# Kernel optimization log

Measured on AMD Instinct MI355X. Metric: run time of the kernel, lower is better.

The kernel has to match this reference:

```python
import jax, jax.numpy as jnp
import numpy as np

STRIDE, PAD, DIL = 1, 1, 1

def setup_inputs() -> dict:
    key = jax.random.key(0)
    k1, k2, k3, k4, k5 = jax.random.split(key, 5)
    B, C, H, W = 4, 64, 96, 96
    Co, kh, kw = 64, 3, 3
    K = kh * kw
    return {
        "input": jax.random.normal(k1, (B, C, H, W), dtype=jnp.float32),
        "offset": jax.random.normal(k2, (B, 2 * K, H, W), dtype=jnp.float32),
        "mask": jax.random.uniform(k3, (B, K, H, W), dtype=jnp.float32),
        "weight": jax.random.normal(k4, (Co, C, kh, kw), dtype=jnp.float32) * 0.05,
        "bias": jax.random.normal(k5, (Co,), dtype=jnp.float32),
    }


def _dcnv2(input, offset, mask, weight, bias):
    B, C, H, W = input.shape
    Co, Ci, kh, kw = weight.shape
    K = kh * kw
    G = offset.shape[1] // (2 * K)  # deformable groups
    Cg = C // G
    Ho = (H + 2 * PAD - DIL * (kh - 1) - 1) // STRIDE + 1
    Wo = (W + 2 * PAD - DIL * (kw - 1) - 1) // STRIDE + 1

    # offsets stored as (dy, dx) pairs per kernel tap, per group
    off = offset.reshape(B, G, K, 2, Ho, Wo)
    dy, dx = off[:, :, :, 0], off[:, :, :, 1]          # [B,G,K,Ho,Wo]
    m = mask.reshape(B, G, K, Ho, Wo)

    ky = (jnp.arange(K, dtype=jnp.float32) // kw) * DIL
    kx = (jnp.arange(K, dtype=jnp.float32) % kw) * DIL
    by = jnp.arange(Ho, dtype=jnp.float32) * STRIDE - PAD
    bx = jnp.arange(Wo, dtype=jnp.float32) * STRIDE - PAD
    py = dy + ky[None, None, :, None, None] + by[None, None, None, :, None]
    px = dx + kx[None, None, :, None, None] + bx[None, None, None, None, :]

    fy, fx = jnp.floor(py), jnp.floor(px)
    wy, wx = py - fy, px - fx                          # bilinear weights
    iy0, ix0 = fy.astype(jnp.int32), fx.astype(jnp.int32)

    img = input.reshape(B * G, Cg, H * W)

    def gather(iy, ix):
        valid = ((iy >= 0) & (iy < H) & (ix >= 0) & (ix < W)).astype(input.dtype)
        idx = jnp.clip(iy, 0, H - 1) * W + jnp.clip(ix, 0, W - 1)  # [B,G,K,Ho,Wo]
        idxf = idx.reshape(B * G, K * Ho * Wo)
        vals = jax.vmap(lambda a, i: a[:, i])(img, idxf)  # [B*G,Cg,K*Ho*Wo]
        vals = vals.reshape(B, G, Cg, K, Ho, Wo)
        return vals * valid.reshape(B, G, 1, K, Ho, Wo)

    v00 = gather(iy0, ix0)
    v01 = gather(iy0, ix0 + 1)
    v10 = gather(iy0 + 1, ix0)
    v11 = gather(iy0 + 1, ix0 + 1)

    wy_ = wy[:, :, None]  # [B,G,1,K,Ho,Wo]
    wx_ = wx[:, :, None]
    samp = (v00 * (1 - wy_) * (1 - wx_) + v01 * (1 - wy_) * wx_
            + v10 * wy_ * (1 - wx_) + v11 * wy_ * wx_)
    samp = samp * m[:, :, None]                        # modulation

    cols = samp.reshape(B, C, K, Ho, Wo)               # im2col columns
    out = jnp.einsum('bckhw,ock->bohw', cols, weight.reshape(Co, Ci, K))
    return out + bias[None, :, None, None]


def reference(input, offset, mask, weight, bias):
    return _dcnv2(input, offset, mask, weight, bias)
```

## Files before the change

kernel.cpp:

```cpp
#include <hip/hip_runtime.h>

#define Bn  4
#define Cn  64
#define Hn  96
#define Wn  96
#define Con 64
#define Kk  9
#define HW  (Hn*Wn)
#define PIX 16
#define CK  (Cn*Kk)
#define NTILE (HW/PIX)

typedef __attribute__((ext_vector_type(8))) short bf16x8;
typedef __attribute__((ext_vector_type(8))) unsigned short u16x8;
typedef __attribute__((ext_vector_type(4))) float f32x4;

static __device__ __forceinline__ float bf2f(ushort u) {
    return __uint_as_float(((unsigned int)u) << 16);
}
static __device__ __forceinline__ ushort f2bf(float f) {
    unsigned int u = __float_as_uint(f);
    u += 0x7FFFu + ((u >> 16) & 1u);
    return (ushort)(u >> 16);
}

static __device__ __forceinline__ bf16x8 blend8(
    float w00, float w01, float w10, float w11,
    u16x8 g00, u16x8 g01, u16x8 g10, u16x8 g11)
{
    u16x8 r;
    #pragma unroll
    for (int j = 0; j < 8; ++j) {
        const float v = w00 * bf2f(g00[j]) + w01 * bf2f(g01[j])
                      + w10 * bf2f(g10[j]) + w11 * bf2f(g11[j]);
        r[j] = f2bf(v);
    }
    return __builtin_bit_cast(bf16x8, r);
}

__global__ __launch_bounds__(256) void dcnv2_prep(
    const float* __restrict__ in, const float* __restrict__ w,
    ushort* __restrict__ nhwc, ushort* __restrict__ wb2)
{
    const int t = threadIdx.x;
    if (blockIdx.x < 576) {
        __shared__ ushort tile[64][66];
        const int bid = blockIdx.x;
        const int b  = bid / 144;
        const int s0 = (bid % 144) * 64;
        const float* ib = in + (size_t)b * Cn * HW;
        #pragma unroll
        for (int i = 0; i < 16; ++i) {
            const int c = i * 4 + (t >> 6);
            tile[t & 63][c] = f2bf(ib[(size_t)c * HW + s0 + (t & 63)]);
        }
        __syncthreads();
        ushort* ob = nhwc + ((size_t)b * HW + s0) * 64;
        #pragma unroll
        for (int i = 0; i < 16; ++i) {
            const int s = i * 4 + (t >> 6);
            ob[s * 64 + (t & 63)] = tile[s][t & 63];
        }
    } else {
        const int e = (blockIdx.x - 576) * 256 + t;
        if (e < Con * CK) {
            const int j  = e & 7;
            const int l  = (e >> 3) & 63;
            const int sk = e >> 9;
            const int s  = sk / 18;
            const int kk = sk - s * 18;
            const int o  = s * 16 + (l & 15);
            const int ck = kk * 32 + (l >> 4) * 8 + j;
            const int kt = ck >> 6;
            const int c  = ck & 63;
            wb2[e] = f2bf(w[(size_t)o * CK + c * Kk + kt]);
        }
    }
}

__global__ __launch_bounds__(192) void dcnv2_main(
    const ushort* __restrict__ nhwc,
    const ushort* __restrict__ wb2,
    const float*  __restrict__ offset,
    const float*  __restrict__ mask,
    const float*  __restrict__ bias,
    float* __restrict__ out)
{
    __shared__ u16x8 stage[3][512];
    __shared__ float red[2][64][20];

    const int t    = threadIdx.x;
    const int lane = t & 63;
    const int u    = t >> 6;
    const int orig = blockIdx.x;
    const int tile = (orig & 7) * 288 + (orig >> 3);
    const int b    = tile / NTILE;
    const int t16  = tile % NTILE;
    const int pix0 = t16 * PIX;
    const int ho   = pix0 / Wn;
    const int wo0  = pix0 % Wn;
    const int px   = lane & 15;
    const int q    = lane >> 4;
    const int px8  = lane >> 3;
    const int jj   = lane & 7;
    const int fpx  = px & 7;
    const int wo   = wo0 + px;
    const int sp   = ho * Wn + wo;

    const float* __restrict__ obp = offset + (size_t)b * 2 * Kk * HW + sp;
    const float* __restrict__ mbp = mask   + (size_t)b * Kk * HW + sp;
    float dyv[3], dxv[3], mmv[3];
    #pragma unroll
    for (int j = 0; j < 3; ++j) {
        const int k = u * 3 + j;
        dyv[j] = obp[(size_t)(2 * k) * HW];
        dxv[j] = obp[(size_t)(2 * k + 1) * HW];
        mmv[j] = mbp[(size_t)k * HW];
    }

    const ushort* __restrict__ nb = nhwc + (size_t)b * HW * 64;
    const ushort* __restrict__ wl = wb2 + lane * 8;

    f32x4 acc0 = {0.f,0.f,0.f,0.f}, acc1 = {0.f,0.f,0.f,0.f};
    f32x4 acc2 = {0.f,0.f,0.f,0.f}, acc3 = {0.f,0.f,0.f,0.f};

    #pragma unroll
    for (int j = 0; j < 3; ++j) {
        const int k = u * 3 + j;
        const float py  = dyv[j] + (float)u + (float)(ho - 1);
        const float pxf = dxv[j] + (float)j + (float)(wo - 1);
        const float fy = floorf(py), fx = floorf(pxf);
        const int iy0 = (int)fy, ix0 = (int)fx;
        const int iy1 = iy0 + 1, ix1 = ix0 + 1;
        const float wy = py - fy, wx = pxf - fx;
        const float vy0 = (iy0 >= 0 && iy0 < Hn) ? 1.f : 0.f;
        const float vy1 = (iy1 >= 0 && iy1 < Hn) ? 1.f : 0.f;
        const float vx0 = (ix0 >= 0 && ix0 < Wn) ? 1.f : 0.f;
        const float vx1 = (ix1 >= 0 && ix1 < Wn) ? 1.f : 0.f;
        const int cy0 = min(max(iy0, 0), Hn - 1), cy1 = min(max(iy1, 0), Hn - 1);
        const int cx0 = min(max(ix0, 0), Wn - 1), cx1 = min(max(ix1, 0), Wn - 1);
        const float m = mmv[j];
        const float w00 = m * (1.f - wy) * (1.f - wx) * vy0 * vx0;
        const float w01 = m * (1.f - wy) * wx         * vy0 * vx1;
        const float w10 = m * wy         * (1.f - wx) * vy1 * vx0;
        const float w11 = m * wy         * wx         * vy1 * vx1;
        const int ac0 = (cy0 * Wn + cx0) * 64;
        const int ac1 = (cy0 * Wn + cx1) * 64;
        const int ac2 = (cy1 * Wn + cx0) * 64;
        const int ac3 = (cy1 * Wn + cx1) * 64;

        #pragma unroll
        for (int c = 0; c < 4; ++c) {
            const int a = (c == 0) ? ac0 : (c == 1) ? ac1 : (c == 2) ? ac2 : ac3;
            #pragma unroll
            for (int hh = 0; hh < 2; ++hh) {
                const int p    = px8 + hh * 8;
                const int base = __shfl(a, p);
                const u16x8 g  = *(const u16x8*)(nb + base + jj * 8);
                stage[u][(p * 4 + c) * 8 + (jj ^ (p & 7))] = g;
            }
        }

        const ushort* wk = wl + (size_t)(2 * k) * 512;
        const bf16x8 af0a = *(const bf16x8*)(wk);
        const bf16x8 af0b = *(const bf16x8*)(wk + 512);
        const bf16x8 af1a = *(const bf16x8*)(wk + 18 * 512);
        const bf16x8 af1b = *(const bf16x8*)(wk + 19 * 512);
        const bf16x8 af2a = *(const bf16x8*)(wk + 36 * 512);
        const bf16x8 af2b = *(const bf16x8*)(wk + 37 * 512);
        const bf16x8 af3a = *(const bf16x8*)(wk + 54 * 512);
        const bf16x8 af3b = *(const bf16x8*)(wk + 55 * 512);

        const int E0 = px * 4 + 0, E1 = px * 4 + 1, E2 = px * 4 + 2, E3 = px * 4 + 3;
        const u16x8 ga0 = stage[u][E0 * 8 + (q ^ fpx)];
        const u16x8 ga1 = stage[u][E1 * 8 + (q ^ fpx)];
        const u16x8 ga2 = stage[u][E2 * 8 + (q ^ fpx)];
        const u16x8 ga3 = stage[u][E3 * 8 + (q ^ fpx)];
        const u16x8 gb0 = stage[u][E0 * 8 + ((q + 4) ^ fpx)];
        const u16x8 gb1 = stage[u][E1 * 8 + ((q + 4) ^ fpx)];
        const u16x8 gb2 = stage[u][E2 * 8 + ((q + 4) ^ fpx)];
        const u16x8 gb3 = stage[u][E3 * 8 + ((q + 4) ^ fpx)];

        const bf16x8 bfa = blend8(w00, w01, w10, w11, ga0, ga1, ga2, ga3);
        const bf16x8 bfb = blend8(w00, w01, w10, w11, gb0, gb1, gb2, gb3);

        acc0 = __builtin_amdgcn_mfma_f32_16x16x32_bf16(af0a, bfa, acc0, 0, 0, 0);
        acc0 = __builtin_amdgcn_mfma_f32_16x16x32_bf16(af0b, bfb, acc0, 0, 0, 0);
        acc1 = __builtin_amdgcn_mfma_f32_16x16x32_bf16(af1a, bfa, acc1, 0, 0, 0);
        acc1 = __builtin_amdgcn_mfma_f32_16x16x32_bf16(af1b, bfb, acc1, 0, 0, 0);
        acc2 = __builtin_amdgcn_mfma_f32_16x16x32_bf16(af2a, bfa, acc2, 0, 0, 0);
        acc2 = __builtin_amdgcn_mfma_f32_16x16x32_bf16(af2b, bfb, acc2, 0, 0, 0);
        acc3 = __builtin_amdgcn_mfma_f32_16x16x32_bf16(af3a, bfa, acc3, 0, 0, 0);
        acc3 = __builtin_amdgcn_mfma_f32_16x16x32_bf16(af3b, bfb, acc3, 0, 0, 0);
    }

    if (u > 0) {
        float* rp = &red[u - 1][lane][0];
        *(f32x4*)(rp + 0)  = acc0;
        *(f32x4*)(rp + 4)  = acc1;
        *(f32x4*)(rp + 8)  = acc2;
        *(f32x4*)(rp + 12) = acc3;
    }
    __syncthreads();
    if (u == 0) {
        float* __restrict__ op = out + (size_t)b * Con * HW + pix0 + px;
        const float* rp0 = &red[0][lane][0];
        const float* rp1 = &red[1][lane][0];
        const int orow = q * 4;
        #pragma unroll
        for (int s = 0; s < 4; ++s) {
            f32x4 a;
            if (s == 0) a = acc0; else if (s == 1) a = acc1;
            else if (s == 2) a = acc2; else a = acc3;
            const f32x4 r0 = *(const f32x4*)(rp0 + s * 4);
            const f32x4 r1 = *(const f32x4*)(rp1 + s * 4);
            const f32x4 bv = *(const f32x4*)&bias[s * 16 + orow];
            #pragma unroll
            for (int r = 0; r < 4; ++r)
                op[(size_t)(s * 16 + orow + r) * HW] = a[r] + r0[r] + r1[r] + bv[r];
        }
    }
}

__global__ __launch_bounds__(256) void dcnv2_fused(
    const float* __restrict__ input, const float* __restrict__ offset,
    const float* __restrict__ mask, const float* __restrict__ weight,
    const float* __restrict__ bias, float* __restrict__ out)
{
    __shared__ float s_w[PIX*Kk][4];
    __shared__ int   s_a[PIX*Kk][4];
    __shared__ float s_samp[CK*PIX];
    const int t = threadIdx.x, blk = blockIdx.x;
    const int b = blk / NTILE, tile = blk % NTILE;
    const int pix0 = tile * PIX, ho = pix0 / Wn, wo0 = pix0 % Wn;
    if (t < PIX*Kk) {
        const int p = t / Kk, k = t - p*Kk, wo = wo0 + p, sp = ho*Wn + wo;
        const float dy = offset[(size_t)(b*2*Kk + 2*k)*HW + sp];
        const float dx = offset[(size_t)(b*2*Kk + 2*k + 1)*HW + sp];
        const float m  = mask[(size_t)(b*Kk + k)*HW + sp];
        const float py = dy + (float)(k/3) + (float)(ho - 1);
        const float px = dx + (float)(k%3) + (float)(wo - 1);
        const float fy = floorf(py), fx = floorf(px);
        const int iy0 = (int)fy, ix0 = (int)fx, iy1 = iy0+1, ix1 = ix0+1;
        const float wy = py - fy, wx = px - fx;
        const float vy0 = (iy0>=0 && iy0<Hn)?1.f:0.f, vy1 = (iy1>=0 && iy1<Hn)?1.f:0.f;
        const float vx0 = (ix0>=0 && ix0<Wn)?1.f:0.f, vx1 = (ix1>=0 && ix1<Wn)?1.f:0.f;
        const int cy0 = min(max(iy0,0),Hn-1), cy1 = min(max(iy1,0),Hn-1);
        const int cx0 = min(max(ix0,0),Wn-1), cx1 = min(max(ix1,0),Wn-1);
        s_w[t][0]=m*(1.f-wy)*(1.f-wx)*vy0*vx0; s_w[t][1]=m*(1.f-wy)*wx*vy0*vx1;
        s_w[t][2]=m*wy*(1.f-wx)*vy1*vx0;       s_w[t][3]=m*wy*wx*vy1*vx1;
        s_a[t][0]=cy0*Wn+cx0; s_a[t][1]=cy0*Wn+cx1; s_a[t][2]=cy1*Wn+cx0; s_a[t][3]=cy1*Wn+cx1;
    }
    __syncthreads();
    {
        const float* inb = input + (size_t)b*Cn*HW;
        #pragma unroll 4
        for (int e = t; e < CK*PIX; e += 256) {
            const int ck = e >> 4, p = e & 15, c = ck / 9, k = ck - c*9, pk = p*Kk + k;
            const float* ic = inb + (size_t)c*HW;
            s_samp[ck*PIX + p] = s_w[pk][0]*ic[s_a[pk][0]] + s_w[pk][1]*ic[s_a[pk][1]]
                               + s_w[pk][2]*ic[s_a[pk][2]] + s_w[pk][3]*ic[s_a[pk][3]];
        }
    }
    __syncthreads();
    const int o = t & 63, pg = t >> 6;
    const float4* wrow = (const float4*)(weight + (size_t)o*CK);
    float ax=0.f, ay=0.f, az=0.f, aw=0.f;
    #pragma unroll 4
    for (int qq = 0; qq < CK/4; ++qq) {
        const float4 wv = wrow[qq];
        const float4 s0 = *(const float4*)&s_samp[(4*qq+0)*PIX + pg*4];
        const float4 s1 = *(const float4*)&s_samp[(4*qq+1)*PIX + pg*4];
        const float4 s2 = *(const float4*)&s_samp[(4*qq+2)*PIX + pg*4];
        const float4 s3 = *(const float4*)&s_samp[(4*qq+3)*PIX + pg*4];
        ax += wv.x*s0.x + wv.y*s1.x + wv.z*s2.x + wv.w*s3.x;
        ay += wv.x*s0.y + wv.y*s1.y + wv.z*s2.y + wv.w*s3.y;
        az += wv.x*s0.z + wv.y*s1.z + wv.z*s2.z + wv.w*s3.z;
        aw += wv.x*s0.w + wv.y*s1.w + wv.z*s2.w + wv.w*s3.w;
    }
    const float bo = bias[o];
    float* op = out + (size_t)(b*Con + o)*HW + pix0 + pg*4;
    op[0]=ax+bo; op[1]=ay+bo; op[2]=az+bo; op[3]=aw+bo;
}

extern "C" void kernel_launch(void* const* d_in, const int* in_sizes, int n_in,
                              void* d_out, int out_size, void* d_ws, size_t ws_size,
                              hipStream_t stream) {
    const float* input  = (const float*)d_in[0];
    const float* offset = (const float*)d_in[1];
    const float* mask   = (const float*)d_in[2];
    const float* weight = (const float*)d_in[3];
    const float* bias   = (const float*)d_in[4];
    float* out = (float*)d_out;

    const size_t nhwc_bytes = (size_t)Bn * HW * 64 * 2;
    const size_t wb_bytes   = (size_t)Con * CK * 2;
    if (ws_size >= nhwc_bytes + wb_bytes) {
        ushort* nhwc = (ushort*)d_ws;
        ushort* wbuf = (ushort*)((char*)d_ws + nhwc_bytes);
        hipLaunchKernelGGL(dcnv2_prep, dim3(720), dim3(256), 0, stream,
                           input, weight, nhwc, wbuf);
        hipLaunchKernelGGL(dcnv2_main, dim3(Bn * NTILE), dim3(192), 0, stream,
                           nhwc, wbuf, offset, mask, bias, out);
    } else {
        hipLaunchKernelGGL(dcnv2_fused, dim3(Bn * NTILE), dim3(256), 0, stream,
                           input, offset, mask, weight, bias, out);
    }
}
```

Before: 28.08 us.

## Process two pixel tiles per block, reusing register-resident weight fragments

Each block of dcnv2_main now handles two adjacent 16-pixel tiles instead of one, halving the grid to 1152 blocks. All bf16 weight fragments for the block's three kernel taps are loaded once into registers up front and reused for both tiles, which removes the repeated per-tile weight loads from global memory. An amdgpu_waves_per_eu(2,2) attribute is added to steer register allocation. The trade-offs are higher register pressure, a larger reduction buffer in shared memory, and fewer blocks, which may leave fewer waves resident to hide the gather latency.

```diff
diff --git a/kernel.cpp b/kernel.cpp
--- a/kernel.cpp
+++ b/kernel.cpp
@@ -78,7 +78,9 @@
     }
 }
 
-__global__ __launch_bounds__(192) void dcnv2_main(
+__global__ __launch_bounds__(192)
+__attribute__((amdgpu_waves_per_eu(2, 2)))
+void dcnv2_main(
     const ushort* __restrict__ nhwc,
     const ushort* __restrict__ wb2,
     const float*  __restrict__ offset,
@@ -87,15 +89,16 @@
     float* __restrict__ out)
 {
     __shared__ u16x8 stage[3][512];
-    __shared__ float red[2][64][20];
+    __shared__ float red[2][2][64][20];
 
     const int t    = threadIdx.x;
     const int lane = t & 63;
     const int u    = t >> 6;
     const int orig = blockIdx.x;
-    const int tile = (orig & 7) * 288 + (orig >> 3);
-    const int b    = tile / NTILE;
-    const int t16  = tile % NTILE;
+    const int pair = (orig & 7) * 144 + (orig >> 3);
+    const int tile0 = pair * 2;
+    const int b    = tile0 / NTILE;
+    const int t16  = tile0 % NTILE;
     const int pix0 = t16 * PIX;
     const int ho   = pix0 / Wn;
     const int wo0  = pix0 % Wn;
@@ -104,120 +107,151 @@
     const int px8  = lane >> 3;
     const int jj   = lane & 7;
     const int fpx  = px & 7;
-    const int wo   = wo0 + px;
-    const int sp   = ho * Wn + wo;
-
-    const float* __restrict__ obp = offset + (size_t)b * 2 * Kk * HW + sp;
-    const float* __restrict__ mbp = mask   + (size_t)b * Kk * HW + sp;
-    float dyv[3], dxv[3], mmv[3];
+
+    const float* __restrict__ obase = offset + (size_t)b * 2 * Kk * HW;
+    const float* __restrict__ mbase = mask   + (size_t)b * Kk * HW;
+    float dyv[2][3], dxv[2][3], mmv[2][3];
+    #pragma unroll
+    for (int tt = 0; tt < 2; ++tt) {
+        const int sp = ho * Wn + wo0 + tt * 16 + px;
+        #pragma unroll
+        for (int j = 0; j < 3; ++j) {
+            const int k = u * 3 + j;
+            dyv[tt][j] = obase[(size_t)(2 * k) * HW + sp];
+            dxv[tt][j] = obase[(size_t)(2 * k + 1) * HW + sp];
+            mmv[tt][j] = mbase[(size_t)k * HW + sp];
+        }
+    }
+
+    const ushort* __restrict__ wl = wb2 + lane * 8;
+    bf16x8 wf[3][2][4];
     #pragma unroll
     for (int j = 0; j < 3; ++j) {
-        const int k = u * 3 + j;
-        dyv[j] = obp[(size_t)(2 * k) * HW];
-        dxv[j] = obp[(size_t)(2 * k + 1) * HW];
-        mmv[j] = mbp[(size_t)k * HW];
-    }
+        const int kk0 = 2 * (u * 3 + j);
+        #pragma unroll
+        for (int h = 0; h < 2; ++h) {
+            #pragma unroll
+            for (int s = 0; s < 4; ++s)
+                wf[j][h][s] = *(const bf16x8*)(wl + (size_t)(s * 18 + kk0 + h) * 512);
+        }
+    }
+    #pragma unroll
+    for (int j = 0; j < 3; ++j)
+        #pragma unroll
+        for (int h = 0; h < 2; ++h)
+            #pragma unroll
+            for (int s = 0; s < 4; ++s)
+                asm volatile("" : "+v"(wf[j][h][s]));
 
     const ushort* __restrict__ nb = nhwc + (size_t)b * HW * 64;
-    const ushort* __restrict__ wl = wb2 + lane * 8;
-
-    f32x4 acc0 = {0.f,0.f,0.f,0.f}, acc1 = {0.f,0.f,0.f,0.f};
-    f32x4 acc2 = {0.f,0.f,0.f,0.f}, acc3 = {0.f,0.f,0.f,0.f};
-
-    #pragma unroll
-    for (int j = 0; j < 3; ++j) {
-        const int k = u * 3 + j;
-        const float py  = dyv[j] + (float)u + (float)(ho - 1);
-        const float pxf = dxv[j] + (float)j + (float)(wo - 1);
-        const float fy = floorf(py), fx = floorf(pxf);
-        const int iy0 = (int)fy, ix0 = (int)fx;
-        const int iy1 = iy0 + 1, ix1 = ix0 + 1;
-        const float wy = py - fy, wx = pxf - fx;
-        const float vy0 = (iy0 >= 0 && iy0 < Hn) ? 1.f : 0.f;
-        const float vy1 = (iy1 >= 0 && iy1 < Hn) ? 1.f : 0.f;
-        const float vx0 = (ix0 >= 0 && ix0 < Wn) ? 1.f : 0.f;
-        const float vx1 = (ix1 >= 0 && ix1 < Wn) ? 1.f : 0.f;
-        const int cy0 = min(max(iy0, 0), Hn - 1), cy1 = min(max(iy1, 0), Hn - 1);
-        const int cx0 = min(max(ix0, 0), Wn - 1), cx1 = min(max(ix1, 0), Wn - 1);
-        const float m = mmv[j];
-        const float w00 = m * (1.f - wy) * (1.f - wx) * vy0 * vx0;
-        const float w01 = m * (1.f - wy) * wx         * vy0 * vx1;
-        const float w10 = m * wy         * (1.f - wx) * vy1 * vx0;
-        const float w11 = m * wy         * wx         * vy1 * vx1;
-        const int ac0 = (cy0 * Wn + cx0) * 64;
-        const int ac1 = (cy0 * Wn + cx1) * 64;
-        const int ac2 = (cy1 * Wn + cx0) * 64;
-        const int ac3 = (cy1 * Wn + cx1) * 64;
-
-        #pragma unroll
-        for (int c = 0; c < 4; ++c) {
-            const int a = (c == 0) ? ac0 : (c == 1) ? ac1 : (c == 2) ? ac2 : ac3;
+
+    f32x4 a0_0 = {0,0,0,0}, a0_1 = {0,0,0,0}, a0_2 = {0,0,0,0}, a0_3 = {0,0,0,0};
+    f32x4 a1_0 = {0,0,0,0}, a1_1 = {0,0,0,0}, a1_2 = {0,0,0,0}, a1_3 = {0,0,0,0};
+
+    #pragma unroll
+    for (int tt = 0; tt < 2; ++tt) {
+        const int wo = wo0 + tt * 16 + px;
+        #pragma unroll
+        for (int j = 0; j < 3; ++j) {
+            const float py  = dyv[tt][j] + (float)u + (float)(ho - 1);
+            const float pxf = dxv[tt][j] + (float)j + (float)(wo - 1);
+            const float fy = floorf(py), fx = floorf(pxf);
+            const int iy0 = (int)fy, ix0 = (int)fx;
+            const int iy1 = iy0 + 1, ix1 = ix0 + 1;
+            const float wy = py - fy, wx = pxf - fx;
+            const float vy0 = (iy0 >= 0 && iy0 < Hn) ? 1.f : 0.f;
+            const float vy1 = (iy1 >= 0 && iy1 < Hn) ? 1.f : 0.f;
+            const float vx0 = (ix0 >= 0 && ix0 < Wn) ? 1.f : 0.f;
+            const float vx1 = (ix1 >= 0 && ix1 < Wn) ? 1.f : 0.f;
+            const int cy0 = min(max(iy0, 0), Hn - 1), cy1 = min(max(iy1, 0), Hn - 1);
+            const int cx0 = min(max(ix0, 0), Wn - 1), cx1 = min(max(ix1, 0), Wn - 1);
+            const float m = mmv[tt][j];
+            const float w00 = m * (1.f - wy) * (1.f - wx) * vy0 * vx0;
+            const float w01 = m * (1.f - wy) * wx         * vy0 * vx1;
+            const float w10 = m * wy         * (1.f - wx) * vy1 * vx0;
+            const float w11 = m * wy         * wx         * vy1 * vx1;
+            const int ac0 = (cy0 * Wn + cx0) * 64;
+            const int ac1 = (cy0 * Wn + cx1) * 64;
+            const int ac2 = (cy1 * Wn + cx0) * 64;
+            const int ac3 = (cy1 * Wn + cx1) * 64;
+
             #pragma unroll
-            for (int hh = 0; hh < 2; ++hh) {
-                const int p    = px8 + hh * 8;
-                const int base = __shfl(a, p);
-                const u16x8 g  = *(const u16x8*)(nb + base + jj * 8);
-                stage[u][(p * 4 + c) * 8 + (jj ^ (p & 7))] = g;
+            for (int c = 0; c < 4; ++c) {
+                const int a = (c == 0) ? ac0 : (c == 1) ? ac1 : (c == 2) ? ac2 : ac3;
+                #pragma unroll
+                for (int hh = 0; hh < 2; ++hh) {
+                    const int p    = px8 + hh * 8;
+                    const int base = __shfl(a, p);
+                    const u16x8 g  = *(const u16x8*)(nb + base + jj * 8);
+                    stage[u][(p * 4 + c) * 8 + (jj ^ (p & 7))] = g;
+                }
             }
-        }
-
-        const ushort* wk = wl + (size_t)(2 * k) * 512;
-        const bf16x8 af0a = *(const bf16x8*)(wk);
-        const bf16x8 af0b = *(const bf16x8*)(wk + 512);
-        const bf16x8 af1a = *(const bf16x8*)(wk + 18 * 512);
-        const bf16x8 af1b = *(const bf16x8*)(wk + 19 * 512);
-        const bf16x8 af2a = *(const bf16x8*)(wk + 36 * 512);
-        const bf16x8 af2b = *(const bf16x8*)(wk + 37 * 512);
-        const bf16x8 af3a = *(const bf16x8*)(wk + 54 * 512);
-        const bf16x8 af3b = *(const bf16x8*)(wk + 55 * 512);
-
-        const int E0 = px * 4 + 0, E1 = px * 4 + 1, E2 = px * 4 + 2, E3 = px * 4 + 3;
-        const u16x8 ga0 = stage[u][E0 * 8 + (q ^ fpx)];
-        const u16x8 ga1 = stage[u][E1 * 8 + (q ^ fpx)];
-        const u16x8 ga2 = stage[u][E2 * 8 + (q ^ fpx)];
-        const u16x8 ga3 = stage[u][E3 * 8 + (q ^ fpx)];
-        const u16x8 gb0 = stage[u][E0 * 8 + ((q + 4) ^ fpx)];
-        const u16x8 gb1 = stage[u][E1 * 8 + ((q + 4) ^ fpx)];
-        const u16x8 gb2 = stage[u][E2 * 8 + ((q + 4) ^ fpx)];
-        const u16x8 gb3 = stage[u][E3 * 8 + ((q + 4) ^ fpx)];
-
-        const bf16x8 bfa = blend8(w00, w01, w10, w11, ga0, ga1, ga2, ga3);
-        const bf16x8 bfb = blend8(w00, w01, w10, w11, gb0, gb1, gb2, gb3);
-
-        acc0 = __builtin_amdgcn_mfma_f32_16x16x32_bf16(af0a, bfa, acc0, 0, 0, 0);
-        acc0 = __builtin_amdgcn_mfma_f32_16x16x32_bf16(af0b, bfb, acc0, 0, 0, 0);
-        acc1 = __builtin_amdgcn_mfma_f32_16x16x32_bf16(af1a, bfa, acc1, 0, 0, 0);
-        acc1 = __builtin_amdgcn_mfma_f32_16x16x32_bf16(af1b, bfb, acc1, 0, 0, 0);
-        acc2 = __builtin_amdgcn_mfma_f32_16x16x32_bf16(af2a, bfa, acc2, 0, 0, 0);
-        acc2 = __builtin_amdgcn_mfma_f32_16x16x32_bf16(af2b, bfb, acc2, 0, 0, 0);
-        acc3 = __builtin_amdgcn_mfma_f32_16x16x32_bf16(af3a, bfa, acc3, 0, 0, 0);
-        acc3 = __builtin_amdgcn_mfma_f32_16x16x32_bf16(af3b, bfb, acc3, 0, 0, 0);
+
+            const int E0 = px * 4 + 0, E1 = px * 4 + 1, E2 = px * 4 + 2, E3 = px * 4 + 3;
+            const u16x8 ga0 = stage[u][E0 * 8 + (q ^ fpx)];
+            const u16x8 ga1 = stage[u][E1 * 8 + (q ^ fpx)];
+            const u16x8 ga2 = stage[u][E2 * 8 + (q ^ fpx)];
+            const u16x8 ga3 = stage[u][E3 * 8 + (q ^ fpx)];
+            const u16x8 gb0 = stage[u][E0 * 8 + ((q + 4) ^ fpx)];
+            const u16x8 gb1 = stage[u][E1 * 8 + ((q + 4) ^ fpx)];
+            const u16x8 gb2 = stage[u][E2 * 8 + ((q + 4) ^ fpx)];
+            const u16x8 gb3 = stage[u][E3 * 8 + ((q + 4) ^ fpx)];
+
+            const bf16x8 bfa = blend8(w00, w01, w10, w11, ga0, ga1, ga2, ga3);
+            const bf16x8 bfb = blend8(w00, w01, w10, w11, gb0, gb1, gb2, gb3);
+
+            if (tt == 0) {
+                a0_0 = __builtin_amdgcn_mfma_f32_16x16x32_bf16(wf[j][0][0], bfa, a0_0, 0, 0, 0);
+                a0_0 = __builtin_amdgcn_mfma_f32_16x16x32_bf16(wf[j][1][0], bfb, a0_0, 0, 0, 0);
+                a0_1 = __builtin_amdgcn_mfma_f32_16x16x32_bf16(wf[j][0][1], bfa, a0_1, 0, 0, 0);
+                a0_1 = __builtin_amdgcn_mfma_f32_16x16x32_bf16(wf[j][1][1], bfb, a0_1, 0, 0, 0);
+                a0_2 = __builtin_amdgcn_mfma_f32_16x16x32_bf16(wf[j][0][2], bfa, a0_2, 0, 0, 0);
+                a0_2 = __builtin_amdgcn_mfma_f32_16x16x32_bf16(wf[j][1][2], bfb, a0_2, 0, 0, 0);
+                a0_3 = __builtin_amdgcn_mfma_f32_16x16x32_bf16(wf[j][0][3], bfa, a0_3, 0, 0, 0);
+                a0_3 = __builtin_amdgcn_mfma_f32_16x16x32_bf16(wf[j][1][3], bfb, a0_3, 0, 0, 0);
+            } else {
+                a1_0 = __builtin_amdgcn_mfma_f32_16x16x32_bf16(wf[j][0][0], bfa, a1_0, 0, 0, 0);
+                a1_0 = __builtin_amdgcn_mfma_f32_16x16x32_bf16(wf[j][1][0], bfb, a1_0, 0, 0, 0);
+                a1_1 = __builtin_amdgcn_mfma_f32_16x16x32_bf16(wf[j][0][1], bfa, a1_1, 0, 0, 0);
+                a1_1 = __builtin_amdgcn_mfma_f32_16x16x32_bf16(wf[j][1][1], bfb, a1_1, 0, 0, 0);
+                a1_2 = __builtin_amdgcn_mfma_f32_16x16x32_bf16(wf[j][0][2], bfa, a1_2, 0, 0, 0);
+                a1_2 = __builtin_amdgcn_mfma_f32_16x16x32_bf16(wf[j][1][2], bfb, a1_2, 0, 0, 0);
+                a1_3 = __builtin_amdgcn_mfma_f32_16x16x32_bf16(wf[j][0][3], bfa, a1_3, 0, 0, 0);
+                a1_3 = __builtin_amdgcn_mfma_f32_16x16x32_bf16(wf[j][1][3], bfb, a1_3, 0, 0, 0);
+            }
+        }
     }
 
     if (u > 0) {
-        float* rp = &red[u - 1][lane][0];
-        *(f32x4*)(rp + 0)  = acc0;
-        *(f32x4*)(rp + 4)  = acc1;
-        *(f32x4*)(rp + 8)  = acc2;
-        *(f32x4*)(rp + 12) = acc3;
+        #pragma unroll
+        for (int tt = 0; tt < 2; ++tt) {
+            float* rp = &red[tt][u - 1][lane][0];
+            *(f32x4*)(rp + 0)  = tt ? a1_0 : a0_0;
+            *(f32x4*)(rp + 4)  = tt ? a1_1 : a0_1;
+            *(f32x4*)(rp + 8)  = tt ? a1_2 : a0_2;
+            *(f32x4*)(rp + 12) = tt ? a1_3 : a0_3;
+        }
     }
     __syncthreads();
     if (u == 0) {
-        float* __restrict__ op = out + (size_t)b * Con * HW + pix0 + px;
-        const float* rp0 = &red[0][lane][0];
-        const float* rp1 = &red[1][lane][0];
         const int orow = q * 4;
         #pragma unroll
-        for (int s = 0; s < 4; ++s) {
-            f32x4 a;
-            if (s == 0) a = acc0; else if (s == 1) a = acc1;
-            else if (s == 2) a = acc2; else a = acc3;
-            const f32x4 r0 = *(const f32x4*)(rp0 + s * 4);
-            const f32x4 r1 = *(const f32x4*)(rp1 + s * 4);
-            const f32x4 bv = *(const f32x4*)&bias[s * 16 + orow];
+        for (int tt = 0; tt < 2; ++tt) {
+            float* __restrict__ op = out + (size_t)b * Con * HW + pix0 + tt * 16 + px;
+            const float* rp0 = &red[tt][0][lane][0];
+            const float* rp1 = &red[tt][1][lane][0];
             #pragma unroll
-            for (int r = 0; r < 4; ++r)
-                op[(size_t)(s * 16 + orow + r) * HW] = a[r] + r0[r] + r1[r] + bv[r];
+            for (int s = 0; s < 4; ++s) {
+                f32x4 a;
+                if (tt == 0) { a = (s == 0) ? a0_0 : (s == 1) ? a0_1 : (s == 2) ? a0_2 : a0_3; }
+                else         { a = (s == 0) ? a1_0 : (s == 1) ? a1_1 : (s == 2) ? a1_2 : a1_3; }
+                const f32x4 r0 = *(const f32x4*)(rp0 + s * 4);
+                const f32x4 r1 = *(const f32x4*)(rp1 + s * 4);
+                const f32x4 bv = *(const f32x4*)&bias[s * 16 + orow];
+                #pragma unroll
+                for (int r = 0; r < 4; ++r)
+                    op[(size_t)(s * 16 + orow + r) * HW] = a[r] + r0[r] + r1[r] + bv[r];
+            }
         }
     }
 }
@@ -300,7 +334,7 @@
         ushort* wbuf = (ushort*)((char*)d_ws + nhwc_bytes);
         hipLaunchKernelGGL(dcnv2_prep, dim3(720), dim3(256), 0, stream,
                            input, weight, nhwc, wbuf);
-        hipLaunchKernelGGL(dcnv2_main, dim3(Bn * NTILE), dim3(192), 0, stream,
+        hipLaunchKernelGGL(dcnv2_main, dim3(1152), dim3(192), 0, stream,
                            nhwc, wbuf, offset, mask, bias, out);
     } else {
         hipLaunchKernelGGL(dcnv2_fused, dim3(Bn * NTILE), dim3(256), 0, stream,
```

After: 32.31 us. 1.15x slower.
